# Optimization experiments

Hardware: AMD Instinct MI355X
Metric: run time of the kernel (lower is better)

## Reference

```python
import jax, jax.numpy as jnp
import numpy as np


def setup_inputs() -> dict:
    key = jax.random.key(0)
    ks = jax.random.split(key, 4)
    B, H, W, C = 4, 64, 64, 256
    d = C // 8
    x = jax.random.normal(ks[0], (B, H, W, C), dtype=jnp.float32)
    # 1x1 conv weights as [C_in, C_out] matrices (Glorot-ish scale)
    Wq = jax.random.normal(ks[1], (C, d), dtype=jnp.float32) * (1.0 / np.sqrt(C))
    Wk = jax.random.normal(ks[2], (C, d), dtype=jnp.float32) * (1.0 / np.sqrt(C))
    Wv = jax.random.normal(ks[3], (C, C), dtype=jnp.float32) * (1.0 / np.sqrt(C))
    bq = jnp.zeros((d,), dtype=jnp.float32)
    bk = jnp.zeros((d,), dtype=jnp.float32)
    bv = jnp.zeros((C,), dtype=jnp.float32)
    gamma = jnp.float32(0.0)  # matches tf.Variable(0.0)
    return {"x": x, "Wq": Wq, "bq": bq, "Wk": Wk, "bk": bk, "Wv": Wv, "bv": bv, "gamma": gamma}


def reference(x, Wq, bq, Wk, bk, Wv, bv, gamma):
    B, H, W, C = x.shape
    N = H * W
    xf = x.reshape(B, N, C)  # spatial tokens
    q = xf @ Wq + bq  # [B, N, d]
    k = xf @ Wk + bk  # [B, N, d]
    v = xf @ Wv + bv  # [B, N, C]
    energy = jnp.einsum("bnd,bmd->bnm", q, k)  # [B, N, N]
    attn = jax.nn.softmax(energy, axis=-1)
    out = jnp.einsum("bnm,bmc->bnc", attn, v).reshape(B, H, W, C)
    return gamma * out + x
```

## Files before the change

### kernel.cpp

```cpp
#include <hip/hip_runtime.h>
#include <hip/hip_bf16.h>

typedef __attribute__((ext_vector_type(8)))  short short8;
typedef __attribute__((ext_vector_type(4)))  float f32x4;
typedef __attribute__((ext_vector_type(16))) float f32x16;
typedef __attribute__((ext_vector_type(4)))  unsigned int u32x4;

#define LOG2E 1.4426950408889634f

static __device__ __forceinline__ unsigned short f2bf(float f) {
    union { float f; unsigned u; } v; v.f = f;
    unsigned r = v.u + 0x7fffu + ((v.u >> 16) & 1u);
    return (unsigned short)(r >> 16);
}
static __device__ __forceinline__ unsigned cvt_pk_bf16(float lo, float hi) {
    unsigned r;
    asm("v_cvt_pk_bf16_f32 %0, %1, %2" : "=v"(r) : "v"(lo), "v"(hi));
    return r;
}
static __device__ __forceinline__ float exp2_hw(float x) {
    float r;
    asm("v_exp_f32 %0, %1" : "=v"(r) : "v"(x));
    return r;
}

__global__ __launch_bounds__(64) void transpose_w(
    const float* __restrict__ Wq, const float* __restrict__ Wk,
    const float* __restrict__ Wv, unsigned short* __restrict__ Wt)
{
    const int c = blockIdx.x;
    const int t = threadIdx.x;
    const float* W; int col, ldw;
    if (c < 32)      { W = Wq; col = c;      ldw = 32;  }
    else if (c < 64) { W = Wk; col = c - 32; ldw = 32;  }
    else             { W = Wv; col = c - 64; ldw = 256; }
    ushort4 o;
    o.x = f2bf(W[(size_t)(4 * t + 0) * ldw + col]);
    o.y = f2bf(W[(size_t)(4 * t + 1) * ldw + col]);
    o.z = f2bf(W[(size_t)(4 * t + 2) * ldw + col]);
    o.w = f2bf(W[(size_t)(4 * t + 3) * ldw + col]);
    *reinterpret_cast<ushort4*>(Wt + (size_t)c * 256 + 4 * t) = o;
}

__global__ __launch_bounds__(256) void proj_kernel(
    const float* __restrict__ x, const unsigned short* __restrict__ Wt,
    const float* __restrict__ bq, const float* __restrict__ bk,
    const float* __restrict__ bv,
    unsigned short* __restrict__ Qb, unsigned short* __restrict__ Kf,
    unsigned short* __restrict__ Vf)
{
    __shared__ unsigned short x_lds[64][264];
    const int tid = threadIdx.x;
    const int M0  = (blockIdx.x >> 1) * 64;
    const int ctb = (blockIdx.x & 1) * 10;

    #pragma unroll
    for (int j = 0; j < 16; ++j) {
        int idx = j * 256 + tid;
        int row = idx >> 6;
        int qc  = idx & 63;
        const float4 v = *reinterpret_cast<const float4*>(x + (size_t)(M0 + row) * 256 + qc * 4);
        ushort4 o;
        o.x = f2bf(v.x); o.y = f2bf(v.y); o.z = f2bf(v.z); o.w = f2bf(v.w);
        *reinterpret_cast<ushort4*>(&x_lds[row][qc * 4]) = o;
    }
    __syncthreads();

    const int w  = tid >> 6;
    const int l  = tid & 63;
    const int lr = l & 15;
    const int lg = l >> 4;

    short8 a[8];
    #pragma unroll
    for (int kk = 0; kk < 8; ++kk)
        a[kk] = *reinterpret_cast<const short8*>(&x_lds[w * 16 + lr][kk * 32 + lg * 8]);

    const int b   = M0 >> 12;
    const int kt  = (M0 & 4095) >> 6;

    for (int ct = ctb; ct < ctb + 10; ++ct) {
        const int col = ct * 16 + lr;
        f32x4 acc = {0.f, 0.f, 0.f, 0.f};
        #pragma unroll
        for (int kk = 0; kk < 8; ++kk) {
            const short8 bfr = *reinterpret_cast<const short8*>(
                Wt + (size_t)col * 256 + kk * 32 + lg * 8);
            acc = __builtin_amdgcn_mfma_f32_16x16x32_bf16(a[kk], bfr, acc, 0, 0, 0);
        }
        const int rbase = M0 + w * 16 + lg * 4;
        if (ct < 2) {
            const float bias = bq[col];
            #pragma unroll
            for (int r = 0; r < 4; ++r)
                Qb[(size_t)(rbase + r) * 32 + col] = f2bf((acc[r] + bias) * LOG2E);
        } else if (ct < 4) {
            const int colp = col - 32;
            const float bias = bk[colp];
            const int dd = colp >> 4, hj = (colp >> 3) & 1, jj = colp & 7;
            #pragma unroll
            for (int r = 0; r < 4; ++r) {
                const int tt = (rbase + r) & 4095;
                const size_t e = (size_t)b * 131072 + (size_t)kt * 2048
                               + (((tt >> 5) & 1) * 2 + dd) * 512
                               + (hj * 32 + (tt & 31)) * 8 + jj;
                Kf[e] = f2bf(acc[r] + bias);
            }
        } else {
            const int colp = col - 64;
            const float bias = bv[colp];
            const int kk_f = w;
            const int hi_v = (lg >> 1) & 1;
            const int j0   = (lg & 1) * 4;
            const size_t e = (size_t)b * 1048576 + (size_t)kt * 16384
                           + (colp >> 5) * 2048 + kk_f * 512
                           + (hi_v * 32 + (colp & 31)) * 8 + j0;
            ushort4 o;
            o.x = f2bf(acc[0] + bias); o.y = f2bf(acc[1] + bias);
            o.z = f2bf(acc[2] + bias); o.w = f2bf(acc[3] + bias);
            *reinterpret_cast<ushort4*>(Vf + e) = o;
        }
    }
}

__global__ __launch_bounds__(128, 2) void attn_kernel(
    const unsigned short* __restrict__ Qb, const unsigned short* __restrict__ Kf,
    const unsigned short* __restrict__ Vf, const float* __restrict__ x,
    const float* __restrict__ gamma_p, float* __restrict__ out)
{
    __shared__ float O_sh[4][16][64];
    __shared__ float l_sh[2][32];

    const int i  = blockIdx.x;
    const int b  = (i & 7) >> 1;
    const int t  = ((i >> 3) << 1) | (i & 1);
    const int qt = t >> 1;
    const int cg = t & 1;

    const int tid = threadIdx.x;
    const int kh  = tid >> 6;
    const int l   = tid & 63;
    const int l5  = l & 31;
    const int hi  = l >> 5;

    const size_t bN = (size_t)b * 4096;
    const int q0 = qt * 32;
    const int c0 = cg * 128;

    const unsigned short* Kfb = Kf + (size_t)b * 131072 + l * 8;
    const unsigned short* Vfb = Vf + (size_t)b * 1048576 + (c0 >> 5) * 2048 + l * 8;

    short8 qb[2];
    #pragma unroll
    for (int dd = 0; dd < 2; ++dd)
        qb[dd] = *reinterpret_cast<const short8*>(
            Qb + (bN + (size_t)(q0 + l5)) * 32 + dd * 16 + hi * 8);

    f32x16 Oa[4];
    #pragma unroll
    for (int ct = 0; ct < 4; ++ct)
        #pragma unroll
        for (int r = 0; r < 16; ++r) Oa[ct][r] = 0.f;
    float lsum0 = 0.f, lsum1 = 0.f;

    f32x16 z;
    #pragma unroll
    for (int r = 0; r < 16; ++r) z[r] = 0.f;

    const int kt0 = kh * 32;

    auto loadK = [&](short8 (&kA)[2][2], int ktg) {
        const unsigned short* kp = Kfb + (size_t)ktg * 2048;
        #pragma unroll
        for (int ks = 0; ks < 2; ++ks)
            #pragma unroll
            for (int dd = 0; dd < 2; ++dd)
                kA[ks][dd] = *reinterpret_cast<const short8*>(kp + (ks * 2 + dd) * 512);
    };

    auto body = [&](short8 (&kcur)[2][2], short8 (&knxt)[2][2], int ktg, int ktgn) {
        const unsigned short* vp = Vfb + (size_t)ktg * 16384;
        short8 vf[2][4];
        #pragma unroll
        for (int kk = 0; kk < 4; ++kk)
            vf[0][kk] = *reinterpret_cast<const short8*>(vp + kk * 512);
        loadK(knxt, ktgn);
        f32x16 p0 = __builtin_amdgcn_mfma_f32_32x32x16_bf16(kcur[0][0], qb[0], z, 0, 0, 0);
        p0        = __builtin_amdgcn_mfma_f32_32x32x16_bf16(kcur[0][1], qb[1], p0, 0, 0, 0);
        f32x16 p1 = __builtin_amdgcn_mfma_f32_32x32x16_bf16(kcur[1][0], qb[0], z, 0, 0, 0);
        p1        = __builtin_amdgcn_mfma_f32_32x32x16_bf16(kcur[1][1], qb[1], p1, 0, 0, 0);
        short8 pa[4];
        #pragma unroll
        for (int ks = 0; ks < 2; ++ks) {
            float e[16];
            #pragma unroll
            for (int r = 0; r < 16; ++r) {
                const float s = (ks == 0) ? p0[r] : p1[r];
                e[r] = exp2_hw(s);
                if (r & 1) lsum1 += e[r]; else lsum0 += e[r];
            }
            unsigned c[8];
            #pragma unroll
            for (int n = 0; n < 8; ++n) c[n] = cvt_pk_bf16(e[2 * n], e[2 * n + 1]);
            #pragma unroll
            for (int k2 = 0; k2 < 2; ++k2) {
                unsigned d0 = c[4 * k2 + 0], d2 = c[4 * k2 + 2];
                unsigned d1 = c[4 * k2 + 1], d3 = c[4 * k2 + 3];
                asm("v_permlane32_swap_b32 %0, %1" : "+v"(d0), "+v"(d2));
                asm("v_permlane32_swap_b32 %0, %1" : "+v"(d1), "+v"(d3));
                u32x4 u = {d0, d1, d2, d3};
                pa[ks * 2 + k2] = __builtin_bit_cast(short8, u);
            }
        }
        #pragma unroll
        for (int ct = 0; ct < 4; ++ct) {
            if (ct < 3) {
                #pragma unroll
                for (int kk = 0; kk < 4; ++kk)
                    vf[(ct + 1) & 1][kk] = *reinterpret_cast<const short8*>(
                        vp + (ct + 1) * 2048 + kk * 512);
            }
            #pragma unroll
            for (int kk = 0; kk < 4; ++kk)
                Oa[ct] = __builtin_amdgcn_mfma_f32_32x32x16_bf16(pa[kk], vf[ct & 1][kk], Oa[ct], 0, 0, 0);
        }
    };

    short8 kA0[2][2], kA1[2][2];
    loadK(kA0, kt0);
    for (int kt = 0; kt < 32; kt += 2) {
        body(kA0, kA1, kt0 + kt, kt0 + kt + 1);
        body(kA1, kA0, kt0 + kt + 1, kt0 + ((kt + 2) & 31));
    }

    float lsum = lsum0 + lsum1;
    lsum += __shfl_xor(lsum, 32);
    if (hi == 0) l_sh[kh][l5] = lsum;
    #pragma unroll
    for (int ct = 0; ct < 4; ++ct)
        if ((ct >> 1) != kh) {
            #pragma unroll
            for (int r = 0; r < 16; ++r)
                O_sh[ct][r][hi * 32 + l5] = Oa[ct][r];
        }
    __syncthreads();

    const float gamma = gamma_p[0];
    #pragma unroll
    for (int ct = 0; ct < 4; ++ct)
        if ((ct >> 1) == kh) {
            #pragma unroll
            for (int r = 0; r < 16; ++r) {
                const int qr = (r & 3) + 8 * (r >> 2) + 4 * hi;
                const float ltot = l_sh[0][qr] + l_sh[1][qr];
                const float osum = Oa[ct][r] + O_sh[ct][r][hi * 32 + l5];
                const size_t idx = (bN + (size_t)(q0 + qr)) * 256 + c0 + ct * 32 + l5;
                out[idx] = gamma * (osum / ltot) + x[idx];
            }
        }
}

extern "C" void kernel_launch(void* const* d_in, const int* in_sizes, int n_in,
                              void* d_out, int out_size, void* d_ws, size_t ws_size,
                              hipStream_t stream) {
    const float* x     = (const float*)d_in[0];
    const float* Wq    = (const float*)d_in[1];
    const float* bq    = (const float*)d_in[2];
    const float* Wk    = (const float*)d_in[3];
    const float* bk    = (const float*)d_in[4];
    const float* Wv    = (const float*)d_in[5];
    const float* bv    = (const float*)d_in[6];
    const float* gamma = (const float*)d_in[7];
    float* out = (float*)d_out;

    unsigned short* Qb = (unsigned short*)d_ws;
    unsigned short* Kf = Qb + (size_t)16384 * 32;
    unsigned short* Vf = Kf + (size_t)16384 * 32;
    unsigned short* Wt = Vf + (size_t)4 * 256 * 4096;

    transpose_w<<<320, 64, 0, stream>>>(Wq, Wk, Wv, Wt);
    proj_kernel<<<512, 256, 0, stream>>>(x, Wt, bq, bk, bv, Qb, Kf, Vf);
    attn_kernel<<<1024, 128, 0, stream>>>(Qb, Kf, Vf, x, gamma, out);
}
```

Before: 89.70 us.

## Restructure attention into 512-thread blocks covering all channels with 4-way key split

The attention kernel now gives each 512-thread block 64 queries and all 256 channels, split across 2 query halves and 4 key quarters. Each score tile's exponentials are therefore computed once for all channels, not repeated per channel group. Partial outputs are reduced through shared memory in four sync rounds, and the epilogue writes vectorized float4 rows. MFMA sections get raised wave priority, and the weight transpose now stores fragments in MFMA order so B-operand loads are contiguous. In exchange, the kernel needs more accumulator registers and more shared memory, and launches fewer blocks.

```diff
diff --git a/kernel.cpp b/kernel.cpp
--- a/kernel.cpp
+++ b/kernel.cpp
@@ -26,24 +26,32 @@
 
 __global__ __launch_bounds__(64) void transpose_w(
     const float* __restrict__ Wq, const float* __restrict__ Wk,
-    const float* __restrict__ Wv, unsigned short* __restrict__ Wt)
+    const float* __restrict__ Wv, unsigned short* __restrict__ Wtf)
 {
-    const int c = blockIdx.x;
-    const int t = threadIdx.x;
-    const float* W; int col, ldw;
-    if (c < 32)      { W = Wq; col = c;      ldw = 32;  }
-    else if (c < 64) { W = Wk; col = c - 32; ldw = 32;  }
-    else             { W = Wv; col = c - 64; ldw = 256; }
-    ushort4 o;
-    o.x = f2bf(W[(size_t)(4 * t + 0) * ldw + col]);
-    o.y = f2bf(W[(size_t)(4 * t + 1) * ldw + col]);
-    o.z = f2bf(W[(size_t)(4 * t + 2) * ldw + col]);
-    o.w = f2bf(W[(size_t)(4 * t + 3) * ldw + col]);
-    *reinterpret_cast<ushort4*>(Wt + (size_t)c * 256 + 4 * t) = o;
+    const int g  = blockIdx.x;
+    const int ct = g >> 3, kk = g & 7;
+    const int l  = threadIdx.x;
+    const int col = ct * 16 + (l & 15);
+    const int k0  = kk * 32 + (l >> 4) * 8;
+    const float* W; int c, ldw;
+    if (col < 32)      { W = Wq; c = col;      ldw = 32;  }
+    else if (col < 64) { W = Wk; c = col - 32; ldw = 32;  }
+    else               { W = Wv; c = col - 64; ldw = 256; }
+    ushort4 o0, o1;
+    o0.x = f2bf(W[(size_t)(k0 + 0) * ldw + c]);
+    o0.y = f2bf(W[(size_t)(k0 + 1) * ldw + c]);
+    o0.z = f2bf(W[(size_t)(k0 + 2) * ldw + c]);
+    o0.w = f2bf(W[(size_t)(k0 + 3) * ldw + c]);
+    o1.x = f2bf(W[(size_t)(k0 + 4) * ldw + c]);
+    o1.y = f2bf(W[(size_t)(k0 + 5) * ldw + c]);
+    o1.z = f2bf(W[(size_t)(k0 + 6) * ldw + c]);
+    o1.w = f2bf(W[(size_t)(k0 + 7) * ldw + c]);
+    *reinterpret_cast<ushort4*>(Wtf + (size_t)g * 512 + l * 8)     = o0;
+    *reinterpret_cast<ushort4*>(Wtf + (size_t)g * 512 + l * 8 + 4) = o1;
 }
 
 __global__ __launch_bounds__(256) void proj_kernel(
-    const float* __restrict__ x, const unsigned short* __restrict__ Wt,
+    const float* __restrict__ x, const unsigned short* __restrict__ Wtf,
     const float* __restrict__ bq, const float* __restrict__ bk,
     const float* __restrict__ bv,
     unsigned short* __restrict__ Qb, unsigned short* __restrict__ Kf,
@@ -85,7 +93,7 @@
         #pragma unroll
         for (int kk = 0; kk < 8; ++kk) {
             const short8 bfr = *reinterpret_cast<const short8*>(
-                Wt + (size_t)col * 256 + kk * 32 + lg * 8);
+                Wtf + ((size_t)ct * 8 + kk) * 512 + l * 8);
             acc = __builtin_amdgcn_mfma_f32_16x16x32_bf16(a[kk], bfr, acc, 0, 0, 0);
         }
         const int rbase = M0 + w * 16 + lg * 4;
@@ -123,42 +131,41 @@
     }
 }
 
-__global__ __launch_bounds__(128, 2) void attn_kernel(
+__global__ __launch_bounds__(512, 2) void attn_kernel(
     const unsigned short* __restrict__ Qb, const unsigned short* __restrict__ Kf,
     const unsigned short* __restrict__ Vf, const float* __restrict__ x,
     const float* __restrict__ gamma_p, float* __restrict__ out)
 {
-    __shared__ float O_sh[4][16][64];
-    __shared__ float l_sh[2][32];
+    __shared__ float Obuf[2][32][260];
+    __shared__ float lbuf[2][4][32];
 
     const int i  = blockIdx.x;
-    const int b  = (i & 7) >> 1;
-    const int t  = ((i >> 3) << 1) | (i & 1);
-    const int qt = t >> 1;
-    const int cg = t & 1;
+    const int b  = i & 3;
+    const int qt = i >> 2;
 
     const int tid = threadIdx.x;
-    const int kh  = tid >> 6;
+    const int w   = tid >> 6;
+    const int qs  = w & 1;
+    const int kh  = w >> 1;
     const int l   = tid & 63;
     const int l5  = l & 31;
     const int hi  = l >> 5;
 
     const size_t bN = (size_t)b * 4096;
-    const int q0 = qt * 32;
-    const int c0 = cg * 128;
+    const int q0 = qt * 64;
 
     const unsigned short* Kfb = Kf + (size_t)b * 131072 + l * 8;
-    const unsigned short* Vfb = Vf + (size_t)b * 1048576 + (c0 >> 5) * 2048 + l * 8;
+    const unsigned short* Vfb = Vf + (size_t)b * 1048576 + l * 8;
 
     short8 qb[2];
     #pragma unroll
     for (int dd = 0; dd < 2; ++dd)
         qb[dd] = *reinterpret_cast<const short8*>(
-            Qb + (bN + (size_t)(q0 + l5)) * 32 + dd * 16 + hi * 8);
-
-    f32x16 Oa[4];
-    #pragma unroll
-    for (int ct = 0; ct < 4; ++ct)
+            Qb + (bN + (size_t)(q0 + qs * 32 + l5)) * 32 + dd * 16 + hi * 8);
+
+    f32x16 Oa[8];
+    #pragma unroll
+    for (int ct = 0; ct < 8; ++ct)
         #pragma unroll
         for (int r = 0; r < 16; ++r) Oa[ct][r] = 0.f;
     float lsum0 = 0.f, lsum1 = 0.f;
@@ -167,7 +174,7 @@
     #pragma unroll
     for (int r = 0; r < 16; ++r) z[r] = 0.f;
 
-    const int kt0 = kh * 32;
+    const int kt0 = kh * 16;
 
     auto loadK = [&](short8 (&kA)[2][2], int ktg) {
         const unsigned short* kp = Kfb + (size_t)ktg * 2048;
@@ -178,6 +185,28 @@
                 kA[ks][dd] = *reinterpret_cast<const short8*>(kp + (ks * 2 + dd) * 512);
     };
 
+    short8 pa[4];
+    auto build_pa = [&](const f32x16& p, int base) {
+        float e[16];
+        #pragma unroll
+        for (int r = 0; r < 16; ++r) {
+            e[r] = exp2_hw(p[r]);
+            if (r & 1) lsum1 += e[r]; else lsum0 += e[r];
+        }
+        unsigned c[8];
+        #pragma unroll
+        for (int n = 0; n < 8; ++n) c[n] = cvt_pk_bf16(e[2 * n], e[2 * n + 1]);
+        #pragma unroll
+        for (int k2 = 0; k2 < 2; ++k2) {
+            unsigned d0 = c[4 * k2 + 0], d2 = c[4 * k2 + 2];
+            unsigned d1 = c[4 * k2 + 1], d3 = c[4 * k2 + 3];
+            asm("v_permlane32_swap_b32 %0, %1" : "+v"(d0), "+v"(d2));
+            asm("v_permlane32_swap_b32 %0, %1" : "+v"(d1), "+v"(d3));
+            u32x4 u = {d0, d1, d2, d3};
+            pa[base + k2] = __builtin_bit_cast(short8, u);
+        }
+    };
+
     auto body = [&](short8 (&kcur)[2][2], short8 (&knxt)[2][2], int ktg, int ktgn) {
         const unsigned short* vp = Vfb + (size_t)ktg * 16384;
         short8 vf[2][4];
@@ -185,36 +214,20 @@
         for (int kk = 0; kk < 4; ++kk)
             vf[0][kk] = *reinterpret_cast<const short8*>(vp + kk * 512);
         loadK(knxt, ktgn);
-        f32x16 p0 = __builtin_amdgcn_mfma_f32_32x32x16_bf16(kcur[0][0], qb[0], z, 0, 0, 0);
-        p0        = __builtin_amdgcn_mfma_f32_32x32x16_bf16(kcur[0][1], qb[1], p0, 0, 0, 0);
-        f32x16 p1 = __builtin_amdgcn_mfma_f32_32x32x16_bf16(kcur[1][0], qb[0], z, 0, 0, 0);
-        p1        = __builtin_amdgcn_mfma_f32_32x32x16_bf16(kcur[1][1], qb[1], p1, 0, 0, 0);
-        short8 pa[4];
-        #pragma unroll
-        for (int ks = 0; ks < 2; ++ks) {
-            float e[16];
-            #pragma unroll
-            for (int r = 0; r < 16; ++r) {
-                const float s = (ks == 0) ? p0[r] : p1[r];
-                e[r] = exp2_hw(s);
-                if (r & 1) lsum1 += e[r]; else lsum0 += e[r];
-            }
-            unsigned c[8];
-            #pragma unroll
-            for (int n = 0; n < 8; ++n) c[n] = cvt_pk_bf16(e[2 * n], e[2 * n + 1]);
-            #pragma unroll
-            for (int k2 = 0; k2 < 2; ++k2) {
-                unsigned d0 = c[4 * k2 + 0], d2 = c[4 * k2 + 2];
-                unsigned d1 = c[4 * k2 + 1], d3 = c[4 * k2 + 3];
-                asm("v_permlane32_swap_b32 %0, %1" : "+v"(d0), "+v"(d2));
-                asm("v_permlane32_swap_b32 %0, %1" : "+v"(d1), "+v"(d3));
-                u32x4 u = {d0, d1, d2, d3};
-                pa[ks * 2 + k2] = __builtin_bit_cast(short8, u);
-            }
-        }
-        #pragma unroll
-        for (int ct = 0; ct < 4; ++ct) {
-            if (ct < 3) {
+        {
+            f32x16 p = __builtin_amdgcn_mfma_f32_32x32x16_bf16(kcur[0][0], qb[0], z, 0, 0, 0);
+            p        = __builtin_amdgcn_mfma_f32_32x32x16_bf16(kcur[0][1], qb[1], p, 0, 0, 0);
+            build_pa(p, 0);
+        }
+        {
+            f32x16 p = __builtin_amdgcn_mfma_f32_32x32x16_bf16(kcur[1][0], qb[0], z, 0, 0, 0);
+            p        = __builtin_amdgcn_mfma_f32_32x32x16_bf16(kcur[1][1], qb[1], p, 0, 0, 0);
+            build_pa(p, 2);
+        }
+        __builtin_amdgcn_s_setprio(1);
+        #pragma unroll
+        for (int ct = 0; ct < 8; ++ct) {
+            if (ct < 7) {
                 #pragma unroll
                 for (int kk = 0; kk < 4; ++kk)
                     vf[(ct + 1) & 1][kk] = *reinterpret_cast<const short8*>(
@@ -224,40 +237,53 @@
             for (int kk = 0; kk < 4; ++kk)
                 Oa[ct] = __builtin_amdgcn_mfma_f32_32x32x16_bf16(pa[kk], vf[ct & 1][kk], Oa[ct], 0, 0, 0);
         }
+        __builtin_amdgcn_s_setprio(0);
     };
 
     short8 kA0[2][2], kA1[2][2];
     loadK(kA0, kt0);
-    for (int kt = 0; kt < 32; kt += 2) {
+    for (int kt = 0; kt < 16; kt += 2) {
         body(kA0, kA1, kt0 + kt, kt0 + kt + 1);
-        body(kA1, kA0, kt0 + kt + 1, kt0 + ((kt + 2) & 31));
-    }
-
-    float lsum = lsum0 + lsum1;
-    lsum += __shfl_xor(lsum, 32);
-    if (hi == 0) l_sh[kh][l5] = lsum;
-    #pragma unroll
-    for (int ct = 0; ct < 4; ++ct)
-        if ((ct >> 1) != kh) {
-            #pragma unroll
-            for (int r = 0; r < 16; ++r)
-                O_sh[ct][r][hi * 32 + l5] = Oa[ct][r];
-        }
-    __syncthreads();
+        body(kA1, kA0, kt0 + kt + 1, kt0 + ((kt + 2) & 15));
+    }
+
+    lsum0 += lsum1;
+    lsum0 += __shfl_xor(lsum0, 32);
+    if (hi == 0) lbuf[qs][kh][l5] = lsum0;
+
+    for (int s = 0; s < 4; ++s) {
+        if (kh == s) {
+            #pragma unroll
+            for (int ct = 0; ct < 8; ++ct)
+                #pragma unroll
+                for (int r = 0; r < 16; ++r) {
+                    const int qr = (r & 3) + 8 * (r >> 2) + 4 * hi;
+                    float* p = &Obuf[qs][qr][ct * 32 + l5];
+                    if (s == 0) *p = Oa[ct][r]; else *p += Oa[ct][r];
+                }
+        }
+        __syncthreads();
+    }
 
     const float gamma = gamma_p[0];
-    #pragma unroll
-    for (int ct = 0; ct < 4; ++ct)
-        if ((ct >> 1) == kh) {
-            #pragma unroll
-            for (int r = 0; r < 16; ++r) {
-                const int qr = (r & 3) + 8 * (r >> 2) + 4 * hi;
-                const float ltot = l_sh[0][qr] + l_sh[1][qr];
-                const float osum = Oa[ct][r] + O_sh[ct][r][hi * 32 + l5];
-                const size_t idx = (bN + (size_t)(q0 + qr)) * 256 + c0 + ct * 32 + l5;
-                out[idx] = gamma * (osum / ltot) + x[idx];
-            }
-        }
+    const int er  = w * 8 + (l >> 3);
+    const int eqs = er >> 5, eq = er & 31;
+    const float ltot = lbuf[eqs][0][eq] + lbuf[eqs][1][eq]
+                     + lbuf[eqs][2][eq] + lbuf[eqs][3][eq];
+    const float linv = gamma / ltot;
+    #pragma unroll
+    for (int it = 0; it < 8; ++it) {
+        const int c4 = (l & 7) + it * 8;
+        const f32x4 o = *reinterpret_cast<const f32x4*>(&Obuf[eqs][eq][c4 * 4]);
+        const size_t idx = (bN + (size_t)(q0 + er)) * 256 + c4 * 4;
+        const float4 xi = *reinterpret_cast<const float4*>(x + idx);
+        float4 ov;
+        ov.x = o[0] * linv + xi.x;
+        ov.y = o[1] * linv + xi.y;
+        ov.z = o[2] * linv + xi.z;
+        ov.w = o[3] * linv + xi.w;
+        *reinterpret_cast<float4*>(out + idx) = ov;
+    }
 }
 
 extern "C" void kernel_launch(void* const* d_in, const int* in_sizes, int n_in,
@@ -273,12 +299,12 @@
     const float* gamma = (const float*)d_in[7];
     float* out = (float*)d_out;
 
-    unsigned short* Qb = (unsigned short*)d_ws;
-    unsigned short* Kf = Qb + (size_t)16384 * 32;
-    unsigned short* Vf = Kf + (size_t)16384 * 32;
-    unsigned short* Wt = Vf + (size_t)4 * 256 * 4096;
-
-    transpose_w<<<320, 64, 0, stream>>>(Wq, Wk, Wv, Wt);
-    proj_kernel<<<512, 256, 0, stream>>>(x, Wt, bq, bk, bv, Qb, Kf, Vf);
-    attn_kernel<<<1024, 128, 0, stream>>>(Qb, Kf, Vf, x, gamma, out);
-}
+    unsigned short* Qb  = (unsigned short*)d_ws;
+    unsigned short* Kf  = Qb + (size_t)16384 * 32;
+    unsigned short* Vf  = Kf + (size_t)16384 * 32;
+    unsigned short* Wtf = Vf + (size_t)4 * 256 * 4096;
+
+    transpose_w<<<160, 64, 0, stream>>>(Wq, Wk, Wv, Wtf);
+    proj_kernel<<<512, 256, 0, stream>>>(x, Wtf, bq, bk, bv, Qb, Kf, Vf);
+    attn_kernel<<<256, 512, 0, stream>>>(Qb, Kf, Vf, x, gamma, out);
+}
```

After: 98.79 us. +10.1%, slower.
